# Kernel tuning notes

Hardware: AMD Instinct MI355X
Metric: run time of the kernel (lower is better)

## Reference

```python
import jax, jax.numpy as jnp
import numpy as np

DG = 8   # deformable groups
KK = 9   # 3x3 kernel positions


def conv3x3(x, w, b):
    # x: [B,C,H,W], w: [O,I,3,3] -> SAME conv, stride 1
    y = jax.lax.conv_general_dilated(x, w, (1, 1), 'SAME',
                                     dimension_numbers=('NCHW', 'OIHW', 'NCHW'))
    return y + b[None, :, None, None]


def modulated_deform_conv(x, offset, mask, w, b):
    # x: [B,C,H,W]; offset: [B,DG,KK,2,H,W] (dy,dx per group/kernel-pos);
    # mask: [B,DG,KK,H,W]; w: [O,C,3,3]; groups=1, stride=1, pad=1, dil=1.
    B, C, H, W = x.shape
    cg = C // DG  # channels per deformable group
    dy = offset[:, :, :, 0]  # [B,DG,KK,H,W]
    dx = offset[:, :, :, 1]
    ky, kx = jnp.meshgrid(jnp.arange(3), jnp.arange(3), indexing='ij')
    ky = (ky.reshape(KK) - 1).astype(x.dtype)  # kernel y offsets (pad=1)
    kx = (kx.reshape(KK) - 1).astype(x.dtype)
    py = dy + jnp.arange(H, dtype=x.dtype).reshape(1, 1, 1, H, 1) + ky.reshape(1, 1, KK, 1, 1)
    px = dx + jnp.arange(W, dtype=x.dtype).reshape(1, 1, 1, 1, W) + kx.reshape(1, 1, KK, 1, 1)
    y0 = jnp.floor(py)
    x0 = jnp.floor(px)
    ly = py - y0  # bilinear fractions
    lx = px - x0
    y0i = y0.astype(jnp.int32)
    x0i = x0.astype(jnp.int32)
    xf = x.reshape(B, DG, cg, H * W)

    def gather(yi, xi):
        # zero padding outside the image (per-corner validity)
        valid = ((yi >= 0) & (yi < H) & (xi >= 0) & (xi < W)).astype(x.dtype)
        idx = jnp.clip(yi, 0, H - 1) * W + jnp.clip(xi, 0, W - 1)  # [B,DG,KK,H,W]
        g = jnp.take_along_axis(xf, idx.reshape(B, DG, 1, KK * H * W), axis=-1)
        return g.reshape(B, DG, cg, KK, H, W) * valid[:, :, None]

    v = (((1 - ly) * (1 - lx))[:, :, None] * gather(y0i, x0i)
         + ((1 - ly) * lx)[:, :, None] * gather(y0i, x0i + 1)
         + (ly * (1 - lx))[:, :, None] * gather(y0i + 1, x0i)
         + (ly * lx)[:, :, None] * gather(y0i + 1, x0i + 1))
    v = (v * mask[:, :, None]).reshape(B, C, KK, H, W)  # modulated im2col
    out = jnp.einsum('bckhw,ock->bohw', v, w.reshape(w.shape[0], C, KK))
    return out + b[None, :, None, None]


def setup_inputs() -> dict:
    key = jax.random.key(0)
    ks = jax.random.split(key, 6)
    B, C, H, W = 8, 64, 128, 128
    f = lambda k, s: jax.random.normal(k, s, dtype=jnp.float32)
    return {
        'cat_fea': f(ks[0], (B, C, H, W)),
        'f_fea': f(ks[1], (B, C, H, W)),
        'w_off2d': f(ks[2], (C, C, 3, 3)) * 0.05,
        'b_off2d': jnp.zeros((C,), jnp.float32),
        'w_coff': f(ks[3], (3 * DG * KK, C, 3, 3)) * 0.01,  # small => near-zero offsets, as in DCNv2Pack init
        'b_coff': jnp.zeros((3 * DG * KK,), jnp.float32),
        'w_dconv': f(ks[4], (C, C, 3, 3)) * 0.05,
        'b_dconv': jnp.zeros((C,), jnp.float32),
    }


def reference(cat_fea, f_fea, w_off2d, b_off2d, w_coff, b_coff, w_dconv, b_dconv):
    # offset1 = self.off2d_1(cat_fea)
    offset_feat = conv3x3(cat_fea, w_off2d, b_off2d)
    # DCNv2Pack: conv_offset on the extra feature, chunk into o1,o2,mask
    off = conv3x3(offset_feat, w_coff, b_coff)  # [B, 3*DG*KK, H, W]
    o1, o2, m = jnp.split(off, 3, axis=1)
    B, _, H, W = off.shape
    # offset = cat(o1,o2); CUDA kernel reads channel ((g*KK+i)*2 + {0:y,1:x})
    offset = jnp.concatenate([o1, o2], axis=1).reshape(B, DG, KK, 2, H, W)
    mask = jax.nn.sigmoid(m).reshape(B, DG, KK, H, W)
    return modulated_deform_conv(f_fea, offset, mask, w_dconv, b_dconv)
```

## Files before the change

### kernel.cpp

```cpp
#include <hip/hip_runtime.h>
#include <math.h>

typedef __attribute__((ext_vector_type(4))) float f32x4;
typedef __attribute__((ext_vector_type(8))) short bf16x8;
typedef __attribute__((ext_vector_type(2))) _Float16 f16x2;
typedef __attribute__((ext_vector_type(8))) _Float16 f16x8;

#define HH 128
#define WW 128
#define HWSZ 16384
#define BHW 131072
#define BB 8

__device__ __forceinline__ float bf2f(ushort u) {
    union { uint i; float f; } x; x.i = ((uint)u) << 16; return x.f;
}
__device__ __forceinline__ ushort f2bf(float f) {
    union { float f; uint i; } x; x.f = f;
    uint r = (x.i + 0x7fffu + ((x.i >> 16) & 1u)) >> 16;
    return (ushort)r;
}
__device__ __forceinline__ ushort f2h_bits(float f) {
    union { _Float16 h; ushort u; } x; x.h = (_Float16)f; return x.u;
}

template<int F16>
__global__ __launch_bounds__(256) void to_gp_k(const float* __restrict__ x,
                                               ushort* __restrict__ y) {
    __shared__ ushort lds[64][66];
    int blk = blockIdx.x;
    int b = blk >> 8;
    int hw0 = (blk & 255) << 6;
    int t = threadIdx.x;
    int lane = t & 63;
    int q = t >> 6;
#pragma unroll
    for (int i = 0; i < 16; i++) {
        int c = i * 4 + q;
        float v = x[((size_t)(b * 64 + c) << 14) + hw0 + lane];
        lds[c][lane] = F16 ? f2h_bits(v) : f2bf(v);
    }
    __syncthreads();
#pragma unroll
    for (int it = 0; it < 2; it++) {
        int id = it * 256 + t;
        int cg = id >> 6;
        int px = id & 63;
        uint pk[4];
#pragma unroll
        for (int j = 0; j < 4; j++)
            pk[j] = (uint)lds[cg * 8 + 2 * j][px] | ((uint)lds[cg * 8 + 2 * j + 1][px] << 16);
        *(uint4*)(y + ((((size_t)b * 8 + cg) << 14) + hw0 + px) * 8) = *(uint4*)pk;
    }
}

template<int F16>
__global__ __launch_bounds__(256) void prep_wa(const float* __restrict__ w,
                                               ushort* __restrict__ wa, int Co, int Co_pad) {
    int idx = blockIdx.x * 256 + threadIdx.x;
    if (idx >= Co_pad * 576) return;
    int co = idx / 576, r = idx % 576;
    int kk = r >> 6, ci = r & 63;
    ushort v = 0;
    if (co < Co) {
        float f = w[(co * 64 + ci) * 9 + kk];
        v = F16 ? f2h_bits(f) : f2bf(f);
    }
    wa[idx] = v;
}

template<int NCO, int MODE>
__global__ __launch_bounds__(256, 3) void conv_gemm2_k(
    const ushort* __restrict__ xt, const ushort* __restrict__ wa,
    const float* __restrict__ bias, ushort* __restrict__ y,
    uint* __restrict__ dyxp, ushort* __restrict__ mpl, int Cout) {
    __shared__ ushort Al[NCO * 64 * 64];
    __shared__ ushort Bt[64 * 64];
    int t = threadIdx.x;
    int orig = blockIdx.x;
    int blk = (orig & 7) * 256 + (orig >> 3);
    int b = blk >> 8;
    int h = (blk >> 1) & 127;
    int w0 = (blk & 1) << 6;
    int lane = t & 63;
    int wv = t >> 6;
    int lg = lane >> 4;
    int lr = lane & 15;
    int rs = (lr & 7) << 4;
    int asw = ((lane & 7) ^ (lane >> 3)) << 4;
    const char* wab = (const char*)wa;

    f32x4 acc[NCO][4];
#pragma unroll
    for (int n = 0; n < NCO; n++)
#pragma unroll
        for (int j = 0; j < 4; j++) acc[n][j] = f32x4{0, 0, 0, 0};

#pragma unroll 1
    for (int kk = 0; kk < 9; kk++) {
        int ky = kk / 3;
        int kx = kk - ky * 3;
        __syncthreads();
#pragma unroll
        for (int a = 0; a < 2 * NCO; a++) {
            int rb = wv * (NCO * 16) + a * 8;
            const char* g = wab + (size_t)(rb + (lane >> 3)) * 1152 + kk * 128 + asw;
            __builtin_amdgcn_global_load_lds(
                (const __attribute__((address_space(1))) void*)g,
                (__attribute__((address_space(3))) void*)((char*)Al + rb * 128),
                16, 0, 0);
        }
        int hy = h + ky - 1;
        int wx = w0 + lane + kx - 1;
        bool val = ((unsigned)hy < 128u) && ((unsigned)wx < 128u);
        uint4 v0 = {0u, 0u, 0u, 0u}, v1 = {0u, 0u, 0u, 0u};
        if (val) {
            const ushort* gb = xt + ((((size_t)b * 8 + wv) << 14) + (hy << 7) + wx) * 8;
            v0 = *(const uint4*)gb;
            v1 = *(const uint4*)(gb + (4ull << 17));
        }
        int swl = (lane & 7) << 4;
        *(uint4*)((char*)Bt + lane * 128 + ((wv * 16) ^ swl)) = v0;
        *(uint4*)((char*)Bt + lane * 128 + (((wv + 4) * 16) ^ swl)) = v1;
        __syncthreads();
#pragma unroll
        for (int n = 0; n < NCO; n++) {
            int ar = n * 64 + wv * 16 + lr;
            bf16x8 a0 = *(const bf16x8*)((char*)Al + ar * 128 + ((lg * 16) ^ rs));
            bf16x8 a1 = *(const bf16x8*)((char*)Al + ar * 128 + ((lg * 16 + 64) ^ rs));
#pragma unroll
            for (int j = 0; j < 4; j++) {
                int pr = j * 16 + lr;
                bf16x8 b0 = *(const bf16x8*)((char*)Bt + pr * 128 + ((lg * 16) ^ rs));
                bf16x8 b1 = *(const bf16x8*)((char*)Bt + pr * 128 + ((lg * 16 + 64) ^ rs));
                acc[n][j] = __builtin_amdgcn_mfma_f32_16x16x32_bf16(a0, b0, acc[n][j], 0, 0, 0);
                acc[n][j] = __builtin_amdgcn_mfma_f32_16x16x32_bf16(a1, b1, acc[n][j], 0, 0, 0);
            }
        }
    }

#pragma unroll
    for (int n = 0; n < NCO; n++) {
        int co_g = n * 64 + wv * 16 + lg * 4;
        if (co_g < Cout) {
            float bs[4];
#pragma unroll
            for (int r = 0; r < 4; r++) bs[r] = bias[co_g + r];
#pragma unroll
            for (int j = 0; j < 4; j++) {
                int pxl = j * 16 + lr;
                int hw = (h << 7) + w0 + pxl;
                int bhw = (b << 14) + hw;
                if (MODE == 0) {
                    int cg = co_g >> 3, cs = co_g & 7;
                    uint2 s2;
                    s2.x = (uint)f2bf(acc[n][j][0] + bs[0]) | ((uint)f2bf(acc[n][j][1] + bs[1]) << 16);
                    s2.y = (uint)f2bf(acc[n][j][2] + bs[2]) | ((uint)f2bf(acc[n][j][3] + bs[3]) << 16);
                    *(uint2*)(y + ((((size_t)b * 8 + cg) << 14) + hw) * 8 + cs) = s2;
                } else if (co_g < 144) {
                    int p0 = co_g >> 1;
                    uint u0 = (uint)f2bf(acc[n][j][0] + bs[0]) | ((uint)f2bf(acc[n][j][1] + bs[1]) << 16);
                    uint u1 = (uint)f2bf(acc[n][j][2] + bs[2]) | ((uint)f2bf(acc[n][j][3] + bs[3]) << 16);
                    dyxp[(size_t)p0 * BHW + bhw] = u0;
                    dyxp[(size_t)(p0 + 1) * BHW + bhw] = u1;
                } else {
#pragma unroll
                    for (int r = 0; r < 4; r++) {
                        float f = 1.f / (1.f + __expf(-(acc[n][j][r] + bs[r])));
                        mpl[(size_t)(co_g - 144 + r) * BHW + bhw] = f2bf(f);
                    }
                }
            }
        }
    }
}

__global__ __launch_bounds__(256, 3) void deform_reg3_k(
    const ushort* __restrict__ xg, const uint* __restrict__ dyxp,
    const ushort* __restrict__ mpl, const ushort* __restrict__ wa,
    const float* __restrict__ bias, float* __restrict__ out) {
    int t = threadIdx.x;
    int orig = blockIdx.x;
    int blk = (orig & 7) * 256 + (orig >> 3);
    int b = blk >> 8;
    int h = (blk >> 1) & 127;
    int w0 = (blk & 1) << 6;
    int lane = t & 63;
    int wv = t >> 6;
    int lg = lane >> 4;
    int lr = lane & 15;
    int wabs = w0 + wv * 16 + lr;
    int bhw = (b << 14) + (h << 7) + wabs;

    uint dyxv[18];
    float mv[18];
#pragma unroll
    for (int c = 0; c < 18; c++) {
        int dg = ((c & 1) << 2) + lg;
        int tap = c >> 1;
        dyxv[c] = dyxp[(size_t)(dg * 9 + tap) * BHW + bhw];
        mv[c] = bf2f(mpl[(size_t)(dg * 9 + tap) * BHW + bhw]);
    }

    uint4 qg[2][4];
    f32x4 wt4[2];
    f16x8 afr[2][4];
    f32x4 acc[4] = {f32x4{0,0,0,0}, f32x4{0,0,0,0}, f32x4{0,0,0,0}, f32x4{0,0,0,0}};

#define DPRE(c) do {                                                            \
    const int tap = (c) >> 1;                                                   \
    const int ky = tap / 3;                                                     \
    const int kx = tap - ky * 3;                                                \
    int dg = (((c) & 1) << 2) + lg;                                             \
    uint dyx = dyxv[(c)];                                                       \
    float dy = bf2f((ushort)(dyx & 0xffff));                                    \
    float dx = bf2f((ushort)(dyx >> 16));                                       \
    float py = dy + (float)(h + ky - 1);                                        \
    float px_ = dx + (float)(wabs + kx - 1);                                    \
    float fy = floorf(py), fx = floorf(px_);                                    \
    int y0 = (int)fy, x0 = (int)fx;                                             \
    int y1 = y0 + 1, x1 = x0 + 1;                                               \
    int y0c = min(max(y0, 0), 127), y1c = min(max(y1, 0), 127);                 \
    int x0c = min(max(x0, 0), 127), x1c = min(max(x1, 0), 127);                 \
    const ushort* gb = xg + (((size_t)b * 8 + dg) << 17);                       \
    qg[(c) & 1][0] = *(const uint4*)(gb + ((y0c << 7) + x0c) * 8);              \
    qg[(c) & 1][1] = *(const uint4*)(gb + ((y0c << 7) + x1c) * 8);              \
    qg[(c) & 1][2] = *(const uint4*)(gb + ((y1c << 7) + x0c) * 8);              \
    qg[(c) & 1][3] = *(const uint4*)(gb + ((y1c << 7) + x1c) * 8);              \
    float ly = py - fy, lx = px_ - fx;                                          \
    bool vy0 = (unsigned)y0 < 128u, vy1 = (unsigned)y1 < 128u;                  \
    bool vx0 = (unsigned)x0 < 128u, vx1 = (unsigned)x1 < 128u;                  \
    float m = mv[(c)];                                                          \
    f32x4 wv4;                                                                  \
    wv4[0] = (vy0 && vx0) ? (1.f - ly) * (1.f - lx) * m : 0.f;                  \
    wv4[1] = (vy0 && vx1) ? (1.f - ly) * lx * m : 0.f;                          \
    wv4[2] = (vy1 && vx0) ? ly * (1.f - lx) * m : 0.f;                          \
    wv4[3] = (vy1 && vx1) ? ly * lx * m : 0.f;                                  \
    wt4[(c) & 1] = wv4;                                                         \
} while (0)

#define APRE(c) do {                                                            \
    const ushort* wac = wa + (c) * 32 + lg * 8;                                 \
    _Pragma("unroll")                                                           \
    for (int n = 0; n < 4; n++)                                                 \
        afr[(c) & 1][n] = *(const f16x8*)(wac + (size_t)(n * 16 + lr) * 576);   \
} while (0)

    DPRE(0);
    APRE(0);

#pragma unroll
    for (int c = 0; c < 18; c++) {
        if (c < 17) {
            DPRE(c + 1);
            APRE(c + 1);
        }
        __builtin_amdgcn_sched_barrier(0);
        f32x4 wc = wt4[c & 1];
        _Float16 wh0 = (_Float16)wc[0], wh1 = (_Float16)wc[1];
        _Float16 wh2 = (_Float16)wc[2], wh3 = (_Float16)wc[3];
        f16x2 w0p = {wh0, wh0}, w1p = {wh1, wh1}, w2p = {wh2, wh2}, w3p = {wh3, wh3};
        union { uint4 u4; uint u[4]; } c00, c01, c10, c11;
        c00.u4 = qg[c & 1][0]; c01.u4 = qg[c & 1][1];
        c10.u4 = qg[c & 1][2]; c11.u4 = qg[c & 1][3];
        union { f16x2 p[4]; f16x8 v; } bf;
#pragma unroll
        for (int c2 = 0; c2 < 4; c2++) {
            union { uint u; f16x2 h; } h00, h01, h10, h11;
            h00.u = c00.u[c2]; h01.u = c01.u[c2];
            h10.u = c10.u[c2]; h11.u = c11.u[c2];
            bf.p[c2] = h00.h * w0p + h01.h * w1p + h10.h * w2p + h11.h * w3p;
        }
#pragma unroll
        for (int n = 0; n < 4; n++)
            acc[n] = __builtin_amdgcn_mfma_f32_16x16x32_f16(afr[c & 1][n], bf.v, acc[n], 0, 0, 0);
    }
#undef DPRE
#undef APRE

    int hw = (h << 7) + wabs;
#pragma unroll
    for (int n = 0; n < 4; n++) {
        int co_g = n * 16 + lg * 4;
#pragma unroll
        for (int r = 0; r < 4; r++) {
            out[((size_t)(b * 64 + co_g + r) << 14) + hw] = acc[n][r] + bias[co_g + r];
        }
    }
}

extern "C" void kernel_launch(void* const* d_in, const int* in_sizes, int n_in,
                              void* d_out, int out_size, void* d_ws, size_t ws_size,
                              hipStream_t stream) {
    const float* cat_fea = (const float*)d_in[0];
    const float* f_fea   = (const float*)d_in[1];
    const float* w_off2d = (const float*)d_in[2];
    const float* b_off2d = (const float*)d_in[3];
    const float* w_coff  = (const float*)d_in[4];
    const float* b_coff  = (const float*)d_in[5];
    const float* w_dconv = (const float*)d_in[6];
    const float* b_dconv = (const float*)d_in[7];
    float* out = (float*)d_out;

    ushort* x1t      = (ushort*)d_ws;
    ushort* xft      = x1t + 8388608;
    ushort* off_feat = xft + 8388608;
    uint*   dyxp     = (uint*)(off_feat + 8388608);
    ushort* mpl      = (ushort*)(dyxp + 9437184);
    ushort* wa1      = mpl + 9437184;
    ushort* wa2      = wa1 + 36864;
    ushort* wad      = wa2 + 147456;

    to_gp_k<0><<<2048, 256, 0, stream>>>(cat_fea, x1t);
    to_gp_k<1><<<2048, 256, 0, stream>>>(f_fea, xft);
    prep_wa<0><<<(64 * 576 + 255) / 256, 256, 0, stream>>>(w_off2d, wa1, 64, 64);
    prep_wa<0><<<(256 * 576 + 255) / 256, 256, 0, stream>>>(w_coff, wa2, 216, 256);
    prep_wa<1><<<(64 * 576 + 255) / 256, 256, 0, stream>>>(w_dconv, wad, 64, 64);

    conv_gemm2_k<1, 0><<<2048, 256, 0, stream>>>(x1t, wa1, b_off2d, off_feat,
                                                 nullptr, nullptr, 64);
    conv_gemm2_k<4, 1><<<2048, 256, 0, stream>>>(off_feat, wa2, b_coff, nullptr,
                                                 dyxp, mpl, 216);
    deform_reg3_k<<<2048, 256, 0, stream>>>(xft, dyxp, mpl, wad, b_dconv, out);
}
```

Before: 184.9 us.

## Split deformable conv into separate sampling pass and MFMA GEMM kernel

Adds a path, taken when the workspace is large enough, that stops fusing bilinear sampling into the deformable-conv GEMM. A sample_k kernel writes the full modulated im2col tensor in bf16 to a workspace buffer, and a simple dgemm_k kernel then runs an MFMA GEMM over it. The goal is to decouple the gather-heavy sampling from the matrix math so each kernel gets better occupancy and simpler scheduling. The cost is roughly 150 MB of extra workspace traffic for the im2col buffer, and the original fused path is kept as a fallback.

Result: faster. 170.3 us (-7.9%).

```diff
diff --git a/kernel.cpp b/kernel.cpp
--- a/kernel.cpp
+++ b/kernel.cpp
@@ -171,6 +171,125 @@
                     }
                 }
             }
+        }
+    }
+}
+
+__global__ __launch_bounds__(256) void sample_k(
+    const ushort* __restrict__ xg, const uint* __restrict__ dyxp,
+    const ushort* __restrict__ mpl, ushort* __restrict__ vt) {
+    int p = blockIdx.y;
+    int dg = p / 9, tap = p - dg * 9;
+    int ky = tap / 3, kx = tap - ky * 3;
+    int bx = blockIdx.x;
+    int bxs = (bx & 7) * 64 + (bx >> 3);
+    int bhw = (bxs << 8) + threadIdx.x;
+    int b = bhw >> 14;
+    int h = (bhw >> 7) & 127;
+    int w = bhw & 127;
+
+    uint dyx = dyxp[(size_t)p * BHW + bhw];
+    float m = bf2f(mpl[(size_t)p * BHW + bhw]);
+    float dy = bf2f((ushort)(dyx & 0xffff));
+    float dx = bf2f((ushort)(dyx >> 16));
+    float py = dy + (float)(h + ky - 1);
+    float px_ = dx + (float)(w + kx - 1);
+    float fy = floorf(py), fx = floorf(px_);
+    int y0 = (int)fy, x0 = (int)fx;
+    int y1 = y0 + 1, x1 = x0 + 1;
+    float ly = py - fy, lx = px_ - fx;
+    bool vy0 = (unsigned)y0 < 128u, vy1 = (unsigned)y1 < 128u;
+    bool vx0 = (unsigned)x0 < 128u, vx1 = (unsigned)x1 < 128u;
+    float w00 = (vy0 && vx0) ? (1.f - ly) * (1.f - lx) * m : 0.f;
+    float w01 = (vy0 && vx1) ? (1.f - ly) * lx * m : 0.f;
+    float w10 = (vy1 && vx0) ? ly * (1.f - lx) * m : 0.f;
+    float w11 = (vy1 && vx1) ? ly * lx * m : 0.f;
+    int y0c = min(max(y0, 0), 127), y1c = min(max(y1, 0), 127);
+    int x0c = min(max(x0, 0), 127), x1c = min(max(x1, 0), 127);
+    const ushort* gb = xg + (((size_t)b * 8 + dg) << 17);
+    uint4 q00 = *(const uint4*)(gb + ((y0c << 7) + x0c) * 8);
+    uint4 q01 = *(const uint4*)(gb + ((y0c << 7) + x1c) * 8);
+    uint4 q10 = *(const uint4*)(gb + ((y1c << 7) + x0c) * 8);
+    uint4 q11 = *(const uint4*)(gb + ((y1c << 7) + x1c) * 8);
+    const ushort* u00 = (const ushort*)&q00;
+    const ushort* u01 = (const ushort*)&q01;
+    const ushort* u10 = (const ushort*)&q10;
+    const ushort* u11 = (const ushort*)&q11;
+    uint pk[4];
+#pragma unroll
+    for (int c2 = 0; c2 < 4; c2++) {
+        float v0 = w00 * bf2f(u00[2*c2])   + w01 * bf2f(u01[2*c2])
+                 + w10 * bf2f(u10[2*c2])   + w11 * bf2f(u11[2*c2]);
+        float v1 = w00 * bf2f(u00[2*c2+1]) + w01 * bf2f(u01[2*c2+1])
+                 + w10 * bf2f(u10[2*c2+1]) + w11 * bf2f(u11[2*c2+1]);
+        pk[c2] = (uint)f2bf(v0) | ((uint)f2bf(v1) << 16);
+    }
+    *(uint4*)(vt + ((size_t)p * BHW + bhw) * 8) = *(uint4*)pk;
+}
+
+__global__ __launch_bounds__(256, 3) void dgemm_k(
+    const ushort* __restrict__ vt, const ushort* __restrict__ wa,
+    const float* __restrict__ bias, float* __restrict__ out) {
+    __shared__ ushort Al[64 * 64];
+    __shared__ ushort Bt[64 * 64];
+    int t = threadIdx.x;
+    int orig = blockIdx.x;
+    int blk = (orig & 7) * 256 + (orig >> 3);
+    int b = blk >> 8;
+    int h = (blk >> 1) & 127;
+    int w0 = (blk & 1) << 6;
+    int lane = t & 63;
+    int wv = t >> 6;
+    int lg = lane >> 4;
+    int lr = lane & 15;
+    int rs = (lr & 7) << 4;
+    int asw = ((lane & 7) ^ (lane >> 3)) << 4;
+    const char* wab = (const char*)wa;
+    int bhw0 = (b << 14) + (h << 7) + w0;
+
+    f32x4 acc[4] = {f32x4{0,0,0,0}, f32x4{0,0,0,0}, f32x4{0,0,0,0}, f32x4{0,0,0,0}};
+
+#pragma unroll 1
+    for (int kk = 0; kk < 9; kk++) {
+        __syncthreads();
+#pragma unroll
+        for (int a = 0; a < 2; a++) {
+            int rb = wv * 16 + a * 8;
+            const char* g = wab + (size_t)(rb + (lane >> 3)) * 1152 + kk * 128 + asw;
+            __builtin_amdgcn_global_load_lds(
+                (const __attribute__((address_space(1))) void*)g,
+                (__attribute__((address_space(3))) void*)((char*)Al + rb * 128),
+                16, 0, 0);
+        }
+        uint4 v0 = *(const uint4*)(vt + ((size_t)(wv * 9 + kk) * BHW + bhw0 + lane) * 8);
+        uint4 v1 = *(const uint4*)(vt + ((size_t)((wv + 4) * 9 + kk) * BHW + bhw0 + lane) * 8);
+        int swl = (lane & 7) << 4;
+        *(uint4*)((char*)Bt + lane * 128 + ((wv * 16) ^ swl)) = v0;
+        *(uint4*)((char*)Bt + lane * 128 + (((wv + 4) * 16) ^ swl)) = v1;
+        __syncthreads();
+        int ar = wv * 16 + lr;
+        bf16x8 a0 = *(const bf16x8*)((char*)Al + ar * 128 + ((lg * 16) ^ rs));
+        bf16x8 a1 = *(const bf16x8*)((char*)Al + ar * 128 + ((lg * 16 + 64) ^ rs));
+#pragma unroll
+        for (int j = 0; j < 4; j++) {
+            int pr = j * 16 + lr;
+            bf16x8 b0 = *(const bf16x8*)((char*)Bt + pr * 128 + ((lg * 16) ^ rs));
+            bf16x8 b1 = *(const bf16x8*)((char*)Bt + pr * 128 + ((lg * 16 + 64) ^ rs));
+            acc[j] = __builtin_amdgcn_mfma_f32_16x16x32_bf16(a0, b0, acc[j], 0, 0, 0);
+            acc[j] = __builtin_amdgcn_mfma_f32_16x16x32_bf16(a1, b1, acc[j], 0, 0, 0);
+        }
+    }
+
+    int co_g = wv * 16 + lg * 4;
+    float bs[4];
+#pragma unroll
+    for (int r = 0; r < 4; r++) bs[r] = bias[co_g + r];
+#pragma unroll
+    for (int j = 0; j < 4; j++) {
+        int hw = (h << 7) + w0 + j * 16 + lr;
+#pragma unroll
+        for (int r = 0; r < 4; r++) {
+            out[((size_t)(b * 64 + co_g + r) << 14) + hw] = acc[j][r] + bs[r];
         }
     }
 }
@@ -302,24 +421,51 @@
     const float* b_dconv = (const float*)d_in[7];
     float* out = (float*)d_out;
 
-    ushort* x1t      = (ushort*)d_ws;
-    ushort* xft      = x1t + 8388608;
-    ushort* off_feat = xft + 8388608;
-    uint*   dyxp     = (uint*)(off_feat + 8388608);
-    ushort* mpl      = (ushort*)(dyxp + 9437184);
-    ushort* wa1      = mpl + 9437184;
-    ushort* wa2      = wa1 + 36864;
-    ushort* wad      = wa2 + 147456;
-
-    to_gp_k<0><<<2048, 256, 0, stream>>>(cat_fea, x1t);
-    to_gp_k<1><<<2048, 256, 0, stream>>>(f_fea, xft);
-    prep_wa<0><<<(64 * 576 + 255) / 256, 256, 0, stream>>>(w_off2d, wa1, 64, 64);
-    prep_wa<0><<<(256 * 576 + 255) / 256, 256, 0, stream>>>(w_coff, wa2, 216, 256);
-    prep_wa<1><<<(64 * 576 + 255) / 256, 256, 0, stream>>>(w_dconv, wad, 64, 64);
-
-    conv_gemm2_k<1, 0><<<2048, 256, 0, stream>>>(x1t, wa1, b_off2d, off_feat,
-                                                 nullptr, nullptr, 64);
-    conv_gemm2_k<4, 1><<<2048, 256, 0, stream>>>(off_feat, wa2, b_coff, nullptr,
-                                                 dyxp, mpl, 216);
-    deform_reg3_k<<<2048, 256, 0, stream>>>(xft, dyxp, mpl, wad, b_dconv, out);
-}
+    const size_t NEED_SG = 224837632ull;
+
+    if (ws_size >= NEED_SG) {
+        ushort* xft  = (ushort*)d_ws;
+        uint*   dyxp = (uint*)(xft + 8388608);
+        ushort* mpl  = (ushort*)(dyxp + 9437184);
+        ushort* wa1  = mpl + 9437184;
+        ushort* wa2  = wa1 + 36864;
+        ushort* wad  = wa2 + 147456;
+        ushort* vt   = wad + 36864;
+        ushort* x1t      = vt;
+        ushort* off_feat = vt + 8388608;
+
+        to_gp_k<0><<<2048, 256, 0, stream>>>(cat_fea, x1t);
+        to_gp_k<0><<<2048, 256, 0, stream>>>(f_fea, xft);
+        prep_wa<0><<<(64 * 576 + 255) / 256, 256, 0, stream>>>(w_off2d, wa1, 64, 64);
+        prep_wa<0><<<(256 * 576 + 255) / 256, 256, 0, stream>>>(w_coff, wa2, 216, 256);
+        prep_wa<0><<<(64 * 576 + 255) / 256, 256, 0, stream>>>(w_dconv, wad, 64, 64);
+
+        conv_gemm2_k<1, 0><<<2048, 256, 0, stream>>>(x1t, wa1, b_off2d, off_feat,
+                                                     nullptr, nullptr, 64);
+        conv_gemm2_k<4, 1><<<2048, 256, 0, stream>>>(off_feat, wa2, b_coff, nullptr,
+                                                     dyxp, mpl, 216);
+        sample_k<<<dim3(512, 72), 256, 0, stream>>>(xft, dyxp, mpl, vt);
+        dgemm_k<<<2048, 256, 0, stream>>>(vt, wad, b_dconv, out);
+    } else {
+        ushort* x1t      = (ushort*)d_ws;
+        ushort* xft      = x1t + 8388608;
+        ushort* off_feat = xft + 8388608;
+        uint*   dyxp     = (uint*)(off_feat + 8388608);
+        ushort* mpl      = (ushort*)(dyxp + 9437184);
+        ushort* wa1      = mpl + 9437184;
+        ushort* wa2      = wa1 + 36864;
+        ushort* wad      = wa2 + 147456;
+
+        to_gp_k<0><<<2048, 256, 0, stream>>>(cat_fea, x1t);
+        to_gp_k<1><<<2048, 256, 0, stream>>>(f_fea, xft);
+        prep_wa<0><<<(64 * 576 + 255) / 256, 256, 0, stream>>>(w_off2d, wa1, 64, 64);
+        prep_wa<0><<<(256 * 576 + 255) / 256, 256, 0, stream>>>(w_coff, wa2, 216, 256);
+        prep_wa<1><<<(64 * 576 + 255) / 256, 256, 0, stream>>>(w_dconv, wad, 64, 64);
+
+        conv_gemm2_k<1, 0><<<2048, 256, 0, stream>>>(x1t, wa1, b_off2d, off_feat,
+                                                     nullptr, nullptr, 64);
+        conv_gemm2_k<4, 1><<<2048, 256, 0, stream>>>(off_feat, wa2, b_coff, nullptr,
+                                                     dyxp, mpl, 216);
+        deform_reg3_k<<<2048, 256, 0, stream>>>(xft, dyxp, mpl, wad, b_dconv, out);
+    }
+}
```
